# Performance work log

Measured on AMD Instinct MI355X. Metric: run time of the kernel, lower is better.

The kernel has to match this reference:

```python
import jax, jax.numpy as jnp
import numpy as np

N_NODES = 100000
N_EDGES = 1200000
IN_CH = 64
HID = 64
OUT_CH = 8
N_GRAPHS = 256


def setup_inputs() -> dict:
    key = jax.random.key(0)
    ks = jax.random.split(key, 12)
    x = jax.random.normal(ks[0], (N_NODES, IN_CH), dtype=jnp.float32)
    edge_index = jax.random.randint(ks[1], (2, N_EDGES), 0, N_NODES, dtype=jnp.int64)
    batch = jnp.sort(jax.random.randint(ks[2], (N_NODES,), 0, N_GRAPHS, dtype=jnp.int64))
    s1 = 1.0 / np.sqrt(IN_CH)
    s2 = 1.0 / np.sqrt(HID)
    # SAGEConv: lin_l (aggregated neighbors, with bias), lin_r (root, no bias)
    W1l = jax.random.uniform(ks[3], (HID, IN_CH), jnp.float32, -s1, s1)
    b1l = jax.random.uniform(ks[4], (HID,), jnp.float32, -s1, s1)
    W1r = jax.random.uniform(ks[5], (HID, IN_CH), jnp.float32, -s1, s1)
    W2l = jax.random.uniform(ks[6], (HID, HID), jnp.float32, -s2, s2)
    b2l = jax.random.uniform(ks[7], (HID,), jnp.float32, -s2, s2)
    W2r = jax.random.uniform(ks[8], (HID, HID), jnp.float32, -s2, s2)
    Wc = jax.random.uniform(ks[9], (OUT_CH, HID), jnp.float32, -s2, s2)
    bc = jax.random.uniform(ks[10], (OUT_CH,), jnp.float32, -s2, s2)
    return {"x": x, "edge_index": edge_index, "batch": batch,
            "W1l": W1l, "b1l": b1l, "W1r": W1r,
            "W2l": W2l, "b2l": b2l, "W2r": W2r,
            "Wc": Wc, "bc": bc}


def _sage_conv(x, src, dst, Wl, bl, Wr):
    # mean aggregation of neighbor (source) features onto targets
    agg = jax.ops.segment_sum(x[src], dst, num_segments=x.shape[0])  # [N, d]
    cnt = jax.ops.segment_sum(jnp.ones((src.shape[0],), x.dtype), dst,
                              num_segments=x.shape[0])
    agg = agg / jnp.maximum(cnt, 1.0)[:, None]
    return agg @ Wl.T + bl + x @ Wr.T


def reference(x, edge_index, batch, W1l, b1l, W1r, W2l, b2l, W2r, Wc, bc):
    src, dst = edge_index[0], edge_index[1]
    h = jax.nn.relu(_sage_conv(x, src, dst, W1l, b1l, W1r))
    # dropout p=0.2 is identity in eval mode
    h = jax.nn.relu(_sage_conv(h, src, dst, W2l, b2l, W2r))
    # global mean pool over graphs
    gsum = jax.ops.segment_sum(h, batch, num_segments=N_GRAPHS)      # [G, HID]
    gcnt = jax.ops.segment_sum(jnp.ones((h.shape[0],), h.dtype), batch,
                               num_segments=N_GRAPHS)
    g = gsum / jnp.maximum(gcnt, 1.0)[:, None]
    return g @ Wc.T + bc
```

## Files before the change

kernel.cpp:

```cpp
#include <hip/hip_runtime.h>

#define N_NODES 100000
#define N_EDGES 1200000
#define CH 64
#define NG 256
#define OC 8
#define NBUK 196
#define BINCHUNK 4096
#define NBLKA 293
#define NSTRIP 6250

typedef unsigned short ushort_t;
typedef unsigned int uint_t;
typedef __attribute__((ext_vector_type(8))) short bf16x8;
typedef __attribute__((ext_vector_type(4))) float f32x4;

__device__ __forceinline__ ushort_t f2bf(float f) {
  uint_t u = __float_as_uint(f);
  return (ushort_t)((u + 0x7FFFu + ((u >> 16) & 1u)) >> 16);
}
__device__ __forceinline__ float bf2f(ushort_t b) {
  return __uint_as_float(((uint_t)b) << 16);
}

__global__ __launch_bounds__(256) void countA_k(const int* __restrict__ dst,
                                                int* __restrict__ gbase) {
  __shared__ int hist[NBUK];
  for (int i = threadIdx.x; i < NBUK; i += 256) hist[i] = 0;
  __syncthreads();
  const int cs = blockIdx.x * BINCHUNK;
  int ce = cs + BINCHUNK;
  if (ce > N_EDGES) ce = N_EDGES;
  for (int e = cs + threadIdx.x; e < ce; e += 256)
    atomicAdd(&hist[dst[e] >> 9], 1);
  __syncthreads();
  for (int b = threadIdx.x; b < NBUK; b += 256) {
    int c = hist[b];
    if (c) atomicAdd(&gbase[b], c);
  }
}

__global__ void scanB_k(const int* __restrict__ gbase, int* __restrict__ boff,
                        int* __restrict__ cursor) {
  __shared__ int s[256];
  int v = (threadIdx.x < NBUK) ? gbase[threadIdx.x] : 0;
  s[threadIdx.x] = v;
  __syncthreads();
  for (int o = 1; o < 256; o <<= 1) {
    int t = (threadIdx.x >= o) ? s[threadIdx.x - o] : 0;
    __syncthreads();
    s[threadIdx.x] += t;
    __syncthreads();
  }
  if (threadIdx.x < NBUK) {
    int ex = s[threadIdx.x] - v;
    boff[threadIdx.x] = ex;
    cursor[threadIdx.x] = ex;
  }
  if (threadIdx.x == NBUK - 1) boff[NBUK] = s[threadIdx.x];
}

__global__ __launch_bounds__(256) void scatterA_k(const int* __restrict__ src,
                                                  const int* __restrict__ dst,
                                                  int* __restrict__ cursor,
                                                  int* __restrict__ tmp) {
  __shared__ int hist[NBUK];
  for (int i = threadIdx.x; i < NBUK; i += 256) hist[i] = 0;
  __syncthreads();
  const int cs = blockIdx.x * BINCHUNK;
  int ce = cs + BINCHUNK;
  if (ce > N_EDGES) ce = N_EDGES;
  for (int e = cs + threadIdx.x; e < ce; e += 256)
    atomicAdd(&hist[dst[e] >> 9], 1);
  __syncthreads();
  for (int b = threadIdx.x; b < NBUK; b += 256) {
    int c = hist[b];
    hist[b] = c ? atomicAdd(&cursor[b], c) : 0;
  }
  __syncthreads();
  for (int e = cs + threadIdx.x; e < ce; e += 256) {
    int d = dst[e];
    int slot = atomicAdd(&hist[d >> 9], 1);
    tmp[slot] = (src[e] << 9) | (d & 511);
  }
}

__global__ __launch_bounds__(512) void csrC_k(const int* __restrict__ tmp,
                                              const int* __restrict__ boff,
                                              int* __restrict__ rp,
                                              int* __restrict__ col) {
  __shared__ int lh[512];
  __shared__ int s[512];
  const int b = blockIdx.x;
  const int tid = threadIdx.x;
  const int eb = boff[b], ee = boff[b + 1];
  lh[tid] = 0;
  __syncthreads();
  for (int e = eb + tid; e < ee; e += 512) atomicAdd(&lh[tmp[e] & 511], 1);
  __syncthreads();
  int v = lh[tid];
  s[tid] = v;
  __syncthreads();
  for (int o = 1; o < 512; o <<= 1) {
    int t = (tid >= o) ? s[tid - o] : 0;
    __syncthreads();
    s[tid] += t;
    __syncthreads();
  }
  const int base = eb + s[tid] - v;
  const int node = b * 512 + tid;
  if (node < N_NODES) rp[node] = base;
  if (b == 0 && tid == 0) rp[N_NODES] = N_EDGES;
  lh[tid] = base;
  __syncthreads();
  for (int e = eb + tid; e < ee; e += 512) {
    int p = tmp[e];
    int slot = atomicAdd(&lh[p & 511], 1);
    col[slot] = p >> 9;
  }
}

__global__ __launch_bounds__(256) void transform_mfma_k(
    const float* in, const float* __restrict__ Wl, const float* __restrict__ Wr,
    ushort_t* __restrict__ outl, float* outr) {
  const int wid = blockIdx.x * 4 + (threadIdx.x >> 6);
  if (wid >= NSTRIP) return;
  const int lane = threadIdx.x & 63;
  const int row = lane & 15;
  const int kb = lane >> 4;

  bf16x8 Bfrag[8][2];
#pragma unroll
  for (int t = 0; t < 8; ++t) {
    const float* W = (t < 4) ? Wl : Wr;
    const int j = (t & 3) * 16 + row;
#pragma unroll
    for (int h = 0; h < 2; ++h) {
      const float* p = W + j * CH + h * 32 + kb * 8;
      float4 w0 = *(const float4*)p;
      float4 w1 = *(const float4*)(p + 4);
      bf16x8 b;
      b[0] = (short)f2bf(w0.x); b[1] = (short)f2bf(w0.y);
      b[2] = (short)f2bf(w0.z); b[3] = (short)f2bf(w0.w);
      b[4] = (short)f2bf(w1.x); b[5] = (short)f2bf(w1.y);
      b[6] = (short)f2bf(w1.z); b[7] = (short)f2bf(w1.w);
      Bfrag[t][h] = b;
    }
  }

  const int n0 = wid * 16;
  bf16x8 Afrag[2];
#pragma unroll
  for (int h = 0; h < 2; ++h) {
    const float* p = in + (size_t)(n0 + row) * CH + h * 32 + kb * 8;
    float4 a0 = *(const float4*)p;
    float4 a1 = *(const float4*)(p + 4);
    bf16x8 a;
    a[0] = (short)f2bf(a0.x); a[1] = (short)f2bf(a0.y);
    a[2] = (short)f2bf(a0.z); a[3] = (short)f2bf(a0.w);
    a[4] = (short)f2bf(a1.x); a[5] = (short)f2bf(a1.y);
    a[6] = (short)f2bf(a1.z); a[7] = (short)f2bf(a1.w);
    Afrag[h] = a;
  }

  f32x4 acc[8];
#pragma unroll
  for (int t = 0; t < 8; ++t) {
    acc[t] = (f32x4){0.f, 0.f, 0.f, 0.f};
    acc[t] = __builtin_amdgcn_mfma_f32_16x16x32_bf16(Afrag[0], Bfrag[t][0],
                                                     acc[t], 0, 0, 0);
    acc[t] = __builtin_amdgcn_mfma_f32_16x16x32_bf16(Afrag[1], Bfrag[t][1],
                                                     acc[t], 0, 0, 0);
  }

  const int orow = (lane >> 4) * 4;
#pragma unroll
  for (int t = 0; t < 4; ++t)
#pragma unroll
    for (int i = 0; i < 4; ++i)
      outl[(size_t)(n0 + orow + i) * CH + t * 16 + row] = f2bf(acc[t][i]);
#pragma unroll
  for (int t = 4; t < 8; ++t)
#pragma unroll
    for (int i = 0; i < 4; ++i)
      outr[(size_t)(n0 + orow + i) * CH + (t - 4) * 16 + row] = acc[t][i];
}

template <int MODE>
__global__ __launch_bounds__(256) void gather_k(
    const ushort_t* __restrict__ gl, const float* gr, const float* __restrict__ bl,
    const int* __restrict__ rowptr, const int* __restrict__ col,
    float* outh, const int* __restrict__ batch,
    float* __restrict__ gsum, int* __restrict__ gcnt) {
  const int lane = threadIdx.x & 63;
  const float biasv = bl[lane];
  const int wid = blockIdx.x * (blockDim.x >> 6) + (threadIdx.x >> 6);
  const int nw = gridDim.x * (blockDim.x >> 6);
  const int per = (N_NODES + nw - 1) / nw;
  int ns = wid * per;
  int ne = ns + per;
  if (ne > N_NODES) ne = N_NODES;
  if (ns >= ne) return;

  int curg = -1;
  float paccv = 0.f;
  int pcnt = 0;

  for (int n = ns; n < ne; ++n) {
    const int eb = rowptr[n], ee = rowptr[n + 1];
    float a0 = 0.f, a1 = 0.f, a2 = 0.f, a3 = 0.f;
    float a4 = 0.f, a5 = 0.f, a6 = 0.f, a7 = 0.f;
    int i = eb;
    for (; i + 8 <= ee; i += 8) {
      int c0 = col[i],     c1 = col[i + 1], c2 = col[i + 2], c3 = col[i + 3];
      int c4 = col[i + 4], c5 = col[i + 5], c6 = col[i + 6], c7 = col[i + 7];
      a0 += bf2f(gl[(size_t)c0 * CH + lane]);
      a1 += bf2f(gl[(size_t)c1 * CH + lane]);
      a2 += bf2f(gl[(size_t)c2 * CH + lane]);
      a3 += bf2f(gl[(size_t)c3 * CH + lane]);
      a4 += bf2f(gl[(size_t)c4 * CH + lane]);
      a5 += bf2f(gl[(size_t)c5 * CH + lane]);
      a6 += bf2f(gl[(size_t)c6 * CH + lane]);
      a7 += bf2f(gl[(size_t)c7 * CH + lane]);
    }
    for (; i + 4 <= ee; i += 4) {
      int c0 = col[i], c1 = col[i + 1], c2 = col[i + 2], c3 = col[i + 3];
      a0 += bf2f(gl[(size_t)c0 * CH + lane]);
      a1 += bf2f(gl[(size_t)c1 * CH + lane]);
      a2 += bf2f(gl[(size_t)c2 * CH + lane]);
      a3 += bf2f(gl[(size_t)c3 * CH + lane]);
    }
    for (; i < ee; ++i) a0 += bf2f(gl[(size_t)col[i] * CH + lane]);
    const int deg = ee - eb;
    const float inv = deg > 0 ? 1.f / (float)deg : 1.f;
    const float s = ((a0 + a1) + (a2 + a3)) + ((a4 + a5) + (a6 + a7));
    const float r =
        fmaxf(fmaf(s, inv, biasv + gr[(size_t)n * CH + lane]), 0.f);
    if (MODE == 0) {
      outh[(size_t)n * CH + lane] = r;
    } else {
      int g = batch[n];
      if (g != curg) {
        if (curg >= 0) {
          atomicAdd(&gsum[curg * CH + lane], paccv);
          if (lane == 0) atomicAdd(&gcnt[curg], pcnt);
        }
        curg = g;
        paccv = 0.f;
        pcnt = 0;
      }
      paccv += r;
      pcnt++;
    }
  }
  if (MODE == 1 && curg >= 0) {
    atomicAdd(&gsum[curg * CH + lane], paccv);
    if (lane == 0) atomicAdd(&gcnt[curg], pcnt);
  }
}

__global__ void final_k(const float* __restrict__ gsum, const int* __restrict__ gcnt,
                        const float* __restrict__ Wc, const float* __restrict__ bc,
                        float* __restrict__ out) {
  __shared__ float Wcs[OC * CH];
  __shared__ float bcs[OC];
  for (int i = threadIdx.x; i < OC * CH; i += blockDim.x) Wcs[i] = Wc[i];
  if (threadIdx.x < OC) bcs[threadIdx.x] = bc[threadIdx.x];
  __syncthreads();
  int g = threadIdx.x;
  float c = (float)gcnt[g];
  float inv = c > 0.f ? 1.f / c : 1.f;
  float gr[CH];
#pragma unroll
  for (int k = 0; k < CH; ++k) gr[k] = gsum[g * CH + k] * inv;
#pragma unroll
  for (int o = 0; o < OC; ++o) {
    float acc = bcs[o];
#pragma unroll
    for (int k = 0; k < CH; ++k) acc += gr[k] * Wcs[o * CH + k];
    out[g * OC + o] = acc;
  }
}

extern "C" void kernel_launch(void* const* d_in, const int* in_sizes, int n_in,
                              void* d_out, int out_size, void* d_ws, size_t ws_size,
                              hipStream_t stream) {
  const float* x   = (const float*)d_in[0];
  const int*   ei  = (const int*)d_in[1];
  const int*   bat = (const int*)d_in[2];
  const float* W1l = (const float*)d_in[3];
  const float* b1l = (const float*)d_in[4];
  const float* W1r = (const float*)d_in[5];
  const float* W2l = (const float*)d_in[6];
  const float* b2l = (const float*)d_in[7];
  const float* W2r = (const float*)d_in[8];
  const float* Wc  = (const float*)d_in[9];
  const float* bc  = (const float*)d_in[10];
  float* out = (float*)d_out;

  char* ws = (char*)d_ws;
  ushort_t* buf1 = (ushort_t*)(ws + 0);
  float* buf2    = (float*)(ws + 25600000);
  int*   tmp     = (int*)(ws + 0);
  int*   rp      = (int*)(ws + 51200000);
  int*   col     = (int*)(ws + 51600128);
  int*   gbase   = (int*)(ws + 56400128);
  int*   boff    = (int*)(ws + 56401152);
  int*   cursor  = (int*)(ws + 56402176);
  float* gsum    = (float*)(ws + 56403200);
  int*   gcnt    = (int*)(ws + 56468736);

  const int* src = ei;
  const int* dst = ei + N_EDGES;

  hipMemsetAsync(gbase, 0, NBUK * sizeof(int), stream);
  hipMemsetAsync(gsum, 0, (size_t)NG * CH * sizeof(float) + NG * sizeof(int), stream);

  countA_k<<<NBLKA, 256, 0, stream>>>(dst, gbase);
  scanB_k<<<1, 256, 0, stream>>>(gbase, boff, cursor);
  scatterA_k<<<NBLKA, 256, 0, stream>>>(src, dst, cursor, tmp);
  csrC_k<<<NBUK, 512, 0, stream>>>(tmp, boff, rp, col);

  transform_mfma_k<<<(NSTRIP + 3) / 4, 256, 0, stream>>>(x, W1l, W1r, buf1, buf2);
  gather_k<0><<<2048, 256, 0, stream>>>(buf1, buf2, b1l, rp, col, buf2,
                                        nullptr, nullptr, nullptr);
  transform_mfma_k<<<(NSTRIP + 3) / 4, 256, 0, stream>>>(buf2, W2l, W2r, buf1, buf2);
  gather_k<1><<<2048, 256, 0, stream>>>(buf1, buf2, b2l, rp, col, nullptr,
                                        bat, gsum, gcnt);
  final_k<<<1, 256, 0, stream>>>(gsum, gcnt, Wc, bc, out);
}
```

Baseline: 232.8 us.

## Store root and hidden features in bf16 and gather packed bf16 pairs

The root-transform output and the layer-1 hidden activations are now stored as bf16 instead of fp32, and the second transform reads bf16 input directly without converting. The gather kernel loads 32-bit words holding two bf16 channels per lane, splits each wavefront into two halves that take alternate edges, and combines the halves with a cross-lane shuffle. This halves the bytes per neighbour row load and the intermediate traffic between stages, in exchange for extra rounding of the root term and hidden state and more shuffle and ALU work per node.

```diff
diff --git a/kernel.cpp b/kernel.cpp
--- a/kernel.cpp
+++ b/kernel.cpp
@@ -19,8 +19,11 @@
   uint_t u = __float_as_uint(f);
   return (ushort_t)((u + 0x7FFFu + ((u >> 16) & 1u)) >> 16);
 }
-__device__ __forceinline__ float bf2f(ushort_t b) {
-  return __uint_as_float(((uint_t)b) << 16);
+__device__ __forceinline__ float bfE(uint_t u) {
+  return __uint_as_float(u << 16);
+}
+__device__ __forceinline__ float bfO(uint_t u) {
+  return __uint_as_float(u & 0xFFFF0000u);
 }
 
 __global__ __launch_bounds__(256) void countA_k(const int* __restrict__ dst,
@@ -120,9 +123,11 @@
   }
 }
 
+template <typename TIN>
 __global__ __launch_bounds__(256) void transform_mfma_k(
-    const float* in, const float* __restrict__ Wl, const float* __restrict__ Wr,
-    ushort_t* __restrict__ outl, float* outr) {
+    const TIN* __restrict__ in, const float* __restrict__ Wl,
+    const float* __restrict__ Wr, ushort_t* __restrict__ outl,
+    ushort_t* __restrict__ outr) {
   const int wid = blockIdx.x * 4 + (threadIdx.x >> 6);
   if (wid >= NSTRIP) return;
   const int lane = threadIdx.x & 63;
@@ -152,15 +157,20 @@
   bf16x8 Afrag[2];
 #pragma unroll
   for (int h = 0; h < 2; ++h) {
-    const float* p = in + (size_t)(n0 + row) * CH + h * 32 + kb * 8;
-    float4 a0 = *(const float4*)p;
-    float4 a1 = *(const float4*)(p + 4);
-    bf16x8 a;
-    a[0] = (short)f2bf(a0.x); a[1] = (short)f2bf(a0.y);
-    a[2] = (short)f2bf(a0.z); a[3] = (short)f2bf(a0.w);
-    a[4] = (short)f2bf(a1.x); a[5] = (short)f2bf(a1.y);
-    a[6] = (short)f2bf(a1.z); a[7] = (short)f2bf(a1.w);
-    Afrag[h] = a;
+    if constexpr (sizeof(TIN) == 4) {
+      const float* p = (const float*)in + (size_t)(n0 + row) * CH + h * 32 + kb * 8;
+      float4 a0 = *(const float4*)p;
+      float4 a1 = *(const float4*)(p + 4);
+      bf16x8 a;
+      a[0] = (short)f2bf(a0.x); a[1] = (short)f2bf(a0.y);
+      a[2] = (short)f2bf(a0.z); a[3] = (short)f2bf(a0.w);
+      a[4] = (short)f2bf(a1.x); a[5] = (short)f2bf(a1.y);
+      a[6] = (short)f2bf(a1.z); a[7] = (short)f2bf(a1.w);
+      Afrag[h] = a;
+    } else {
+      const ushort_t* p = (const ushort_t*)in + (size_t)(n0 + row) * CH + h * 32 + kb * 8;
+      Afrag[h] = *(const bf16x8*)p;
+    }
   }
 
   f32x4 acc[8];
@@ -183,17 +193,20 @@
   for (int t = 4; t < 8; ++t)
 #pragma unroll
     for (int i = 0; i < 4; ++i)
-      outr[(size_t)(n0 + orow + i) * CH + (t - 4) * 16 + row] = acc[t][i];
+      outr[(size_t)(n0 + orow + i) * CH + (t - 4) * 16 + row] = f2bf(acc[t][i]);
 }
 
 template <int MODE>
 __global__ __launch_bounds__(256) void gather_k(
-    const ushort_t* __restrict__ gl, const float* gr, const float* __restrict__ bl,
-    const int* __restrict__ rowptr, const int* __restrict__ col,
-    float* outh, const int* __restrict__ batch,
-    float* __restrict__ gsum, int* __restrict__ gcnt) {
+    const uint_t* __restrict__ glu, const uint_t* __restrict__ gru,
+    const float* __restrict__ bl, const int* __restrict__ rowptr,
+    const int* __restrict__ col, uint_t* __restrict__ outu,
+    const int* __restrict__ batch, float* __restrict__ gsum,
+    int* __restrict__ gcnt) {
   const int lane = threadIdx.x & 63;
-  const float biasv = bl[lane];
+  const int half = lane >> 5;
+  const int cp = lane & 31;
+  const float bE = bl[2 * cp], bO = bl[2 * cp + 1];
   const int wid = blockIdx.x * (blockDim.x >> 6) + (threadIdx.x >> 6);
   const int nw = gridDim.x * (blockDim.x >> 6);
   const int per = (N_NODES + nw - 1) / nw;
@@ -203,58 +216,62 @@
   if (ns >= ne) return;
 
   int curg = -1;
-  float paccv = 0.f;
+  float paccE = 0.f, paccO = 0.f;
   int pcnt = 0;
 
   for (int n = ns; n < ne; ++n) {
     const int eb = rowptr[n], ee = rowptr[n + 1];
-    float a0 = 0.f, a1 = 0.f, a2 = 0.f, a3 = 0.f;
-    float a4 = 0.f, a5 = 0.f, a6 = 0.f, a7 = 0.f;
-    int i = eb;
-    for (; i + 8 <= ee; i += 8) {
-      int c0 = col[i],     c1 = col[i + 1], c2 = col[i + 2], c3 = col[i + 3];
-      int c4 = col[i + 4], c5 = col[i + 5], c6 = col[i + 6], c7 = col[i + 7];
-      a0 += bf2f(gl[(size_t)c0 * CH + lane]);
-      a1 += bf2f(gl[(size_t)c1 * CH + lane]);
-      a2 += bf2f(gl[(size_t)c2 * CH + lane]);
-      a3 += bf2f(gl[(size_t)c3 * CH + lane]);
-      a4 += bf2f(gl[(size_t)c4 * CH + lane]);
-      a5 += bf2f(gl[(size_t)c5 * CH + lane]);
-      a6 += bf2f(gl[(size_t)c6 * CH + lane]);
-      a7 += bf2f(gl[(size_t)c7 * CH + lane]);
-    }
-    for (; i + 4 <= ee; i += 4) {
-      int c0 = col[i], c1 = col[i + 1], c2 = col[i + 2], c3 = col[i + 3];
-      a0 += bf2f(gl[(size_t)c0 * CH + lane]);
-      a1 += bf2f(gl[(size_t)c1 * CH + lane]);
-      a2 += bf2f(gl[(size_t)c2 * CH + lane]);
-      a3 += bf2f(gl[(size_t)c3 * CH + lane]);
-    }
-    for (; i < ee; ++i) a0 += bf2f(gl[(size_t)col[i] * CH + lane]);
+    float e0 = 0.f, o0 = 0.f, e1 = 0.f, o1 = 0.f;
+    float e2 = 0.f, o2 = 0.f, e3 = 0.f, o3 = 0.f;
+    int j = eb + half;
+    for (; j + 6 < ee; j += 8) {
+      int c0 = col[j], c1 = col[j + 2], c4 = col[j + 4], c6 = col[j + 6];
+      uint_t u0 = glu[(size_t)c0 * 32 + cp];
+      uint_t u1 = glu[(size_t)c1 * 32 + cp];
+      uint_t u2 = glu[(size_t)c4 * 32 + cp];
+      uint_t u3 = glu[(size_t)c6 * 32 + cp];
+      e0 += bfE(u0); o0 += bfO(u0);
+      e1 += bfE(u1); o1 += bfO(u1);
+      e2 += bfE(u2); o2 += bfO(u2);
+      e3 += bfE(u3); o3 += bfO(u3);
+    }
+    for (; j < ee; j += 2) {
+      uint_t u = glu[(size_t)col[j] * 32 + cp];
+      e0 += bfE(u); o0 += bfO(u);
+    }
+    float sE = (e0 + e1) + (e2 + e3);
+    float sO = (o0 + o1) + (o2 + o3);
+    sE += __shfl_xor(sE, 32);
+    sO += __shfl_xor(sO, 32);
     const int deg = ee - eb;
     const float inv = deg > 0 ? 1.f / (float)deg : 1.f;
-    const float s = ((a0 + a1) + (a2 + a3)) + ((a4 + a5) + (a6 + a7));
-    const float r =
-        fmaxf(fmaf(s, inv, biasv + gr[(size_t)n * CH + lane]), 0.f);
+    const uint_t ug = gru[(size_t)n * 32 + cp];
+    const float rE = fmaxf(fmaf(sE, inv, bE + bfE(ug)), 0.f);
+    const float rO = fmaxf(fmaf(sO, inv, bO + bfO(ug)), 0.f);
     if (MODE == 0) {
-      outh[(size_t)n * CH + lane] = r;
+      if (half == 0)
+        outu[(size_t)n * 32 + cp] = ((uint_t)f2bf(rO) << 16) | f2bf(rE);
     } else {
       int g = batch[n];
       if (g != curg) {
-        if (curg >= 0) {
-          atomicAdd(&gsum[curg * CH + lane], paccv);
+        if (curg >= 0 && half == 0) {
+          atomicAdd(&gsum[curg * CH + 2 * cp], paccE);
+          atomicAdd(&gsum[curg * CH + 2 * cp + 1], paccO);
           if (lane == 0) atomicAdd(&gcnt[curg], pcnt);
         }
         curg = g;
-        paccv = 0.f;
+        paccE = 0.f;
+        paccO = 0.f;
         pcnt = 0;
       }
-      paccv += r;
+      paccE += rE;
+      paccO += rO;
       pcnt++;
     }
   }
-  if (MODE == 1 && curg >= 0) {
-    atomicAdd(&gsum[curg * CH + lane], paccv);
+  if (MODE == 1 && curg >= 0 && half == 0) {
+    atomicAdd(&gsum[curg * CH + 2 * cp], paccE);
+    atomicAdd(&gsum[curg * CH + 2 * cp + 1], paccO);
     if (lane == 0) atomicAdd(&gcnt[curg], pcnt);
   }
 }
@@ -300,7 +317,8 @@
 
   char* ws = (char*)d_ws;
   ushort_t* buf1 = (ushort_t*)(ws + 0);
-  float* buf2    = (float*)(ws + 25600000);
+  ushort_t* buf3 = (ushort_t*)(ws + 12800000);
+  ushort_t* buf2 = (ushort_t*)(ws + 25600000);
   int*   tmp     = (int*)(ws + 0);
   int*   rp      = (int*)(ws + 51200000);
   int*   col     = (int*)(ws + 51600128);
@@ -321,11 +339,15 @@
   scatterA_k<<<NBLKA, 256, 0, stream>>>(src, dst, cursor, tmp);
   csrC_k<<<NBUK, 512, 0, stream>>>(tmp, boff, rp, col);
 
-  transform_mfma_k<<<(NSTRIP + 3) / 4, 256, 0, stream>>>(x, W1l, W1r, buf1, buf2);
-  gather_k<0><<<2048, 256, 0, stream>>>(buf1, buf2, b1l, rp, col, buf2,
+  transform_mfma_k<float><<<(NSTRIP + 3) / 4, 256, 0, stream>>>(x, W1l, W1r,
+                                                                buf1, buf2);
+  gather_k<0><<<2048, 256, 0, stream>>>((const uint_t*)buf1, (const uint_t*)buf2,
+                                        b1l, rp, col, (uint_t*)buf3,
                                         nullptr, nullptr, nullptr);
-  transform_mfma_k<<<(NSTRIP + 3) / 4, 256, 0, stream>>>(buf2, W2l, W2r, buf1, buf2);
-  gather_k<1><<<2048, 256, 0, stream>>>(buf1, buf2, b2l, rp, col, nullptr,
+  transform_mfma_k<ushort_t><<<(NSTRIP + 3) / 4, 256, 0, stream>>>(buf3, W2l, W2r,
+                                                                   buf1, buf2);
+  gather_k<1><<<2048, 256, 0, stream>>>((const uint_t*)buf1, (const uint_t*)buf2,
+                                        b2l, rp, col, nullptr,
                                         bat, gsum, gcnt);
   final_k<<<1, 256, 0, stream>>>(gsum, gcnt, Wc, bc, out);
 }
```

New measurement: 235.5 us. No clear change (+1.1%).
